# Kernel optimization log

Hardware: AMD Instinct MI355X
Metric: run time of the kernel (lower is better)

## Reference

```python
import jax, jax.numpy as jnp
import numpy as np

EMBED = 768
HEADS = 12


def setup_inputs() -> dict:
    key = jax.random.key(0)
    k1, k2, k3 = jax.random.split(key, 3)
    B, N, E = 2, 2048, EMBED
    x = jax.random.normal(k1, (B, N, E), dtype=jnp.float32)
    w_qkv = jax.random.normal(k2, (3 * E, E), dtype=jnp.float32) * (1.0 / np.sqrt(E))
    b_qkv = jnp.zeros((3 * E,), dtype=jnp.float32)
    w_o = jax.random.normal(k3, (E, E), dtype=jnp.float32) * (1.0 / np.sqrt(E))
    b_o = jnp.zeros((E,), dtype=jnp.float32)
    return {"x": x, "w_qkv": w_qkv, "b_qkv": b_qkv, "w_o": w_o, "b_o": b_o}


def reference(x, w_qkv, b_qkv, w_o, b_o):
    B, N, E = x.shape
    H = HEADS
    d = E // H
    # fused qkv projection (torch Linear: x @ W^T + b)
    qkv = x @ w_qkv.T + b_qkv                       # [B, N, 3E]
    # Rearrange 'b n (h qkv e) -> b qkv h n e'
    qkv = qkv.reshape(B, N, H, 3, d).transpose(0, 3, 2, 1, 4)  # [B, 3, H, N, d]
    q, k, v = qkv[:, 0], qkv[:, 1], qkv[:, 2]       # each [B, H, N, d]
    scores = jnp.einsum("bhqd,bhkd->bhqk", q, k)    # [B, H, N, N]
    attn = jax.nn.softmax(scores / jnp.sqrt(jnp.float32(E)), axis=-1)
    ctx = jnp.einsum("bhqk,bhkd->bhqd", attn, v)    # [B, H, N, d]
    ctx = ctx.transpose(0, 2, 1, 3).reshape(B, N, E)  # 'b h n d -> b n (h d)'
    out = ctx @ w_o.T + b_o
    return out
```

## Files before the change

kernel.cpp:

```cpp
#include <hip/hip_runtime.h>

#define BB 2
#define NN 2048
#define EE 768
#define HH 12
#define DD 64
#define MM (BB*NN)
#define E3 (3*EE)
#define QSCALE 0.05205877280961602f

typedef __bf16 bf16x8 __attribute__((ext_vector_type(8)));
typedef float  f32x4  __attribute__((ext_vector_type(4)));
typedef unsigned short u16x8 __attribute__((ext_vector_type(8)));

#define MFMA(a,b,c) __builtin_amdgcn_mfma_f32_16x16x32_bf16(a,b,c,0,0,0)

__device__ __forceinline__ unsigned short f2bf(float f) {
    unsigned int u = __float_as_uint(f);
    u += 0x7FFFu + ((u >> 16) & 1u);
    return (unsigned short)(u >> 16);
}

typedef __attribute__((address_space(3))) unsigned int as3u32;
typedef __attribute__((address_space(1))) unsigned int as1u32;
__device__ __forceinline__ void gll16(const void* g, void* l) {
    __builtin_amdgcn_global_load_lds((const as1u32*)(uintptr_t)g,
                                     (as3u32*)(unsigned int)(uintptr_t)l, 16, 0, 0);
}

#define XB4 786432
#define WQ4 442368
#define WO4 147456
__global__ __launch_bounds__(256)
void cast3(const float* __restrict__ x, const float* __restrict__ wq,
           const float* __restrict__ wo, unsigned short* __restrict__ dst) {
    int i = blockIdx.x * 256 + threadIdx.x;
    const float* src;
    int off;
    if (i < XB4)            { src = x;  off = i; }
    else if (i < XB4+WQ4)   { src = wq; off = i - XB4; }
    else                    { src = wo; off = i - XB4 - WQ4; }
    float4 v = ((const float4*)src)[off];
    ushort4 o;
    o.x = f2bf(v.x); o.y = f2bf(v.y); o.z = f2bf(v.z); o.w = f2bf(v.w);
    ((ushort4*)dst)[i] = o;
}

__global__ __launch_bounds__(256)
void gemm_qkv(const unsigned short* __restrict__ A, const unsigned short* __restrict__ W,
              const float* __restrict__ bias,
              unsigned short* __restrict__ o0, unsigned short* __restrict__ o1,
              unsigned short* __restrict__ o2)
{
    __shared__ unsigned short As[128 * 32];
    __shared__ unsigned short Bs[64 * 32];

    const int tid = threadIdx.x;
    const int l = tid & 63;
    const int w = tid >> 6;
    const int m0 = blockIdx.x * 128;
    const int c0 = blockIdx.y * 64;
    const int wm = (w >> 1) * 64;
    const int wn = (w & 1) * 32;

    const unsigned short* s_src[3];
    unsigned short* s_dst[3];
    #pragma unroll
    for (int s = 0; s < 3; ++s) {
        const int ch = 3*w + s;
        if (ch < 8) {
            s_src[s] = A + (size_t)(m0 + ch*16 + (l>>2)) * EE + (l&3)*8;
            s_dst[s] = &As[ch*512];
        } else {
            s_src[s] = W + (size_t)(c0 + (ch-8)*16 + (l>>2)) * EE + (l&3)*8;
            s_dst[s] = &Bs[(ch-8)*512];
        }
    }

    const f32x4 zero4 = {0.f, 0.f, 0.f, 0.f};
    f32x4 acc[4][2];
    #pragma unroll
    for (int i = 0; i < 4; ++i)
        #pragma unroll
        for (int j = 0; j < 2; ++j) acc[i][j] = zero4;

    for (int k0 = 0; k0 < EE; k0 += 32) {
        __syncthreads();
        #pragma unroll
        for (int s = 0; s < 3; ++s) gll16(s_src[s] + k0, s_dst[s]);
        __syncthreads();

        bf16x8 af[4], bf[2];
        #pragma unroll
        for (int i = 0; i < 4; ++i)
            af[i] = *(const bf16x8*)&As[(wm + 16*i + (l&15))*32 + (l>>4)*8];
        #pragma unroll
        for (int j = 0; j < 2; ++j)
            bf[j] = *(const bf16x8*)&Bs[(wn + 16*j + (l&15))*32 + (l>>4)*8];
        #pragma unroll
        for (int i = 0; i < 4; ++i)
            #pragma unroll
            for (int j = 0; j < 2; ++j)
                acc[i][j] = MFMA(af[i], bf[j], acc[i][j]);
    }

    const int sec = c0 >> 6;
    const int hh = sec / 3;
    const int tt = sec - hh*3;
    #pragma unroll
    for (int j = 0; j < 2; ++j) {
        const int col = c0 + wn + 16*j + (l&15);
        const int dcol = wn + 16*j + (l&15);
        const float bj = bias[col];
        #pragma unroll
        for (int i = 0; i < 4; ++i) {
            const int row0 = m0 + wm + 16*i + (l>>4)*4;
            const int b = row0 >> 11;
            const int n = row0 & (NN - 1);
            if (tt == 2) {
                ushort4 pk;
                pk.x = f2bf(acc[i][j][0] + bj);
                pk.y = f2bf(acc[i][j][1] + bj);
                pk.z = f2bf(acc[i][j][2] + bj);
                pk.w = f2bf(acc[i][j][3] + bj);
                *(ushort4*)&o2[(((size_t)b*HH + hh)*DD + dcol)*NN + n] = pk;
            } else {
                unsigned short* dst = (tt == 0) ? o0 : o1;
                #pragma unroll
                for (int r = 0; r < 4; ++r) {
                    float val = acc[i][j][r] + bj;
                    if (tt == 0) val *= QSCALE;
                    dst[(((size_t)b*HH + hh)*NN + n + r)*DD + dcol] = f2bf(val);
                }
            }
        }
    }
}

__global__ __launch_bounds__(256)
void gemm_out(const unsigned short* __restrict__ A, const unsigned short* __restrict__ W,
              const float* __restrict__ bias, float* __restrict__ of)
{
    __shared__ unsigned short As[64 * 32];
    __shared__ unsigned short Bs[64 * 32];

    const int tid = threadIdx.x;
    const int l = tid & 63;
    const int w = tid >> 6;
    const int m0 = blockIdx.x * 64;
    const int c0 = blockIdx.y * 64;
    const int wm = (w >> 1) * 32;
    const int wn = (w & 1) * 32;

    const unsigned short* s_src[2];
    unsigned short* s_dst[2];
    #pragma unroll
    for (int s = 0; s < 2; ++s) {
        const int ch = 2*w + s;
        if (ch < 4) {
            s_src[s] = A + (size_t)(m0 + ch*16 + (l>>2)) * EE + (l&3)*8;
            s_dst[s] = &As[ch*512];
        } else {
            s_src[s] = W + (size_t)(c0 + (ch-4)*16 + (l>>2)) * EE + (l&3)*8;
            s_dst[s] = &Bs[(ch-4)*512];
        }
    }

    const f32x4 zero4 = {0.f, 0.f, 0.f, 0.f};
    f32x4 acc[2][2];
    #pragma unroll
    for (int i = 0; i < 2; ++i)
        #pragma unroll
        for (int j = 0; j < 2; ++j) acc[i][j] = zero4;

    for (int k0 = 0; k0 < EE; k0 += 32) {
        __syncthreads();
        #pragma unroll
        for (int s = 0; s < 2; ++s) gll16(s_src[s] + k0, s_dst[s]);
        __syncthreads();

        bf16x8 af[2], bf[2];
        #pragma unroll
        for (int i = 0; i < 2; ++i)
            af[i] = *(const bf16x8*)&As[(wm + 16*i + (l&15))*32 + (l>>4)*8];
        #pragma unroll
        for (int j = 0; j < 2; ++j)
            bf[j] = *(const bf16x8*)&Bs[(wn + 16*j + (l&15))*32 + (l>>4)*8];
        #pragma unroll
        for (int i = 0; i < 2; ++i)
            #pragma unroll
            for (int j = 0; j < 2; ++j)
                acc[i][j] = MFMA(af[i], bf[j], acc[i][j]);
    }

    #pragma unroll
    for (int j = 0; j < 2; ++j) {
        const int col = c0 + wn + 16*j + (l&15);
        const float bj = bias[col];
        #pragma unroll
        for (int i = 0; i < 2; ++i) {
            #pragma unroll
            for (int r = 0; r < 4; ++r) {
                const int row = m0 + wm + 16*i + (l>>4)*4 + r;
                of[(size_t)row * EE + col] = acc[i][j][r] + bj;
            }
        }
    }
}

__global__ __launch_bounds__(256)
void attn_mfma(const unsigned short* __restrict__ Q, const unsigned short* __restrict__ K,
               const unsigned short* __restrict__ Vt_g, unsigned short* __restrict__ ctx)
{
    __shared__ unsigned short Ks[2 * 64 * 64];
    __shared__ unsigned short Vt[2 * 64 * 64];
    __shared__ unsigned short Pq[4 * 2 * 16 * 64];

    const int tid = threadIdx.x;
    const int l = tid & 63;
    const int w = tid >> 6;
    const int quad = l >> 4;
    const int lc = l & 15;
    const int x7 = lc & 7;

    const int id = blockIdx.x;
    const int bh = id % 24;
    const int bq = id / 24;
    const int b  = bh / 12;
    const int h  = bh - b*12;
    const size_t hb = (size_t)bh * NN * DD;

    const f32x4 zero4 = {0.f, 0.f, 0.f, 0.f};

    const int qrow = bq*64 + w*16 + lc;
    const bf16x8 qf0 = *(const bf16x8*)(Q + hb + (size_t)qrow*DD +      quad*8);
    const bf16x8 qf1 = *(const bf16x8*)(Q + hb + (size_t)qrow*DD + 32 + quad*8);

    f32x4 o[4];
    #pragma unroll
    for (int dj = 0; dj < 4; ++dj) o[dj] = zero4;
    float lsum = 0.f;

    const int srow = tid >> 2;
    const int sc = tid & 3;
    const unsigned short* kbase = K + hb + (size_t)srow*DD + sc*16;
    const unsigned short* vbase = Vt_g + hb + (size_t)srow*NN + sc*16;
    const int c0s = ((2*sc)     ^ (srow & 7)) * 8;
    const int c1s = ((2*sc + 1) ^ (srow & 7)) * 8;
    const int so = srow * 64;

    const int chq0 = ((    quad) ^ x7) * 8;
    const int chq1 = ((4 + quad) ^ x7) * 8;
    const int pw = w * 2048;
    const int prd0 = lc*64 + (((    2*quad) ^ (lc & 14)) * 4);
    const int prd1 = lc*64 + (((8 + 2*quad) ^ (lc & 14)) * 4);

    for (int kt = 0; kt < NN/128; ++kt) {
        const unsigned short* k0p = kbase + (size_t)kt*128*DD;
        const unsigned short* k1p = k0p + (size_t)64*DD;
        const unsigned short* v0p = vbase + kt*128;
        const unsigned short* v1p = v0p + 64;
        u16x8 ka0 = *(const u16x8*)k0p;
        u16x8 ka1 = *(const u16x8*)(k0p + 8);
        u16x8 kb0 = *(const u16x8*)k1p;
        u16x8 kb1 = *(const u16x8*)(k1p + 8);
        u16x8 va0 = *(const u16x8*)v0p;
        u16x8 va1 = *(const u16x8*)(v0p + 8);
        u16x8 vb0 = *(const u16x8*)v1p;
        u16x8 vb1 = *(const u16x8*)(v1p + 8);
        __syncthreads();
        *(u16x8*)&Ks[so + c0s] = ka0;
        *(u16x8*)&Ks[so + c1s] = ka1;
        *(u16x8*)&Ks[4096 + so + c0s] = kb0;
        *(u16x8*)&Ks[4096 + so + c1s] = kb1;
        *(u16x8*)&Vt[so + c0s] = va0;
        *(u16x8*)&Vt[so + c1s] = va1;
        *(u16x8*)&Vt[4096 + so + c0s] = vb0;
        *(u16x8*)&Vt[4096 + so + c1s] = vb1;
        __syncthreads();

        #pragma unroll
        for (int hf = 0; hf < 2; ++hf) {
            const int base = hf * 4096;
            const int pb = pw + hf * 1024;

            f32x4 st[4];
            #pragma unroll
            for (int jf = 0; jf < 4; ++jf) {
                bf16x8 kf0 = *(const bf16x8*)&Ks[base + (16*jf + lc)*64 + chq0];
                bf16x8 kf1 = *(const bf16x8*)&Ks[base + (16*jf + lc)*64 + chq1];
                f32x4 acc0 = MFMA(kf0, qf0, zero4);
                st[jf] = MFMA(kf1, qf1, acc0);
            }

            #pragma unroll
            for (int jf = 0; jf < 4; ++jf) {
                float e0 = __builtin_amdgcn_exp2f(st[jf][0]);
                float e1 = __builtin_amdgcn_exp2f(st[jf][1]);
                float e2 = __builtin_amdgcn_exp2f(st[jf][2]);
                float e3 = __builtin_amdgcn_exp2f(st[jf][3]);
                lsum += (e0 + e1) + (e2 + e3);
                ushort4 pk;
                pk.x = f2bf(e0); pk.y = f2bf(e1); pk.z = f2bf(e2); pk.w = f2bf(e3);
                *(ushort4*)&Pq[pb + lc*64 + (((4*jf + quad) ^ (lc & 14)) * 4)] = pk;
            }

            bf16x8 pf0 = *(const bf16x8*)&Pq[pb + prd0];
            bf16x8 pf1 = *(const bf16x8*)&Pq[pb + prd1];
            #pragma unroll
            for (int dj = 0; dj < 4; ++dj) {
                bf16x8 vf0 = *(const bf16x8*)&Vt[base + (16*dj + lc)*64 + chq0];
                bf16x8 vf1 = *(const bf16x8*)&Vt[base + (16*dj + lc)*64 + chq1];
                o[dj] = MFMA(vf0, pf0, o[dj]);
                o[dj] = MFMA(vf1, pf1, o[dj]);
            }
        }
    }

    lsum += __shfl_xor(lsum, 16);
    lsum += __shfl_xor(lsum, 32);
    const float inv = 1.f / lsum;

    const int n = bq*64 + w*16 + lc;
    #pragma unroll
    for (int dj = 0; dj < 4; ++dj) {
        ushort4 pk;
        pk.x = f2bf(o[dj][0] * inv);
        pk.y = f2bf(o[dj][1] * inv);
        pk.z = f2bf(o[dj][2] * inv);
        pk.w = f2bf(o[dj][3] * inv);
        *(ushort4*)&ctx[((size_t)(b*NN + n))*EE + h*DD + 16*dj + quad*4] = pk;
    }
}

extern "C" void kernel_launch(void* const* d_in, const int* in_sizes, int n_in,
                              void* d_out, int out_size, void* d_ws, size_t ws_size,
                              hipStream_t stream)
{
    const float* x     = (const float*)d_in[0];
    const float* w_qkv = (const float*)d_in[1];
    const float* b_qkv = (const float*)d_in[2];
    const float* w_o   = (const float*)d_in[3];
    const float* b_o   = (const float*)d_in[4];
    float* out = (float*)d_out;

    unsigned short* wsu = (unsigned short*)d_ws;
    const size_t XB = (size_t)MM * EE;
    const size_t WQ = (size_t)E3 * EE;
    const size_t WO = (size_t)EE * EE;
    const size_t HS = (size_t)BB * HH * NN * DD;
    unsigned short* xb   = wsu;
    unsigned short* wqb  = xb  + XB;
    unsigned short* wob  = wqb + WQ;
    unsigned short* qb   = wob + WO;
    unsigned short* kb   = qb  + HS;
    unsigned short* vtb  = kb  + HS;
    unsigned short* ctxb = vtb + HS;

    cast3<<<(XB4 + WQ4 + WO4)/256, 256, 0, stream>>>(x, w_qkv, w_o, xb);

    dim3 g1(MM/128, E3/64);
    gemm_qkv<<<g1, 256, 0, stream>>>(xb, wqb, b_qkv, qb, kb, vtb);

    attn_mfma<<<768, 256, 0, stream>>>(qb, kb, vtb, ctxb);

    dim3 g3(MM/64, EE/64);
    gemm_out<<<g3, 256, 0, stream>>>(ctxb, wob, b_o, out);
}
```

Measured before the change: 163.6 us.

## Software-pipeline K/V tile loads into registers across attention iterations

```diff
diff --git a/kernel.cpp b/kernel.cpp
--- a/kernel.cpp
+++ b/kernel.cpp
@@ -208,6 +208,8 @@
     }
 }
 
+struct KVT { u16x8 k0, k1, k2, k3, v0, v1, v2, v3; };
+
 __global__ __launch_bounds__(256)
 void attn_mfma(const unsigned short* __restrict__ Q, const unsigned short* __restrict__ K,
                const unsigned short* __restrict__ Vt_g, unsigned short* __restrict__ ctx)
@@ -255,29 +257,37 @@
     const int prd0 = lc*64 + (((    2*quad) ^ (lc & 14)) * 4);
     const int prd1 = lc*64 + (((8 + 2*quad) ^ (lc & 14)) * 4);
 
-    for (int kt = 0; kt < NN/128; ++kt) {
+    auto loadt = [&](KVT& R, int kt) {
         const unsigned short* k0p = kbase + (size_t)kt*128*DD;
-        const unsigned short* k1p = k0p + (size_t)64*DD;
         const unsigned short* v0p = vbase + kt*128;
-        const unsigned short* v1p = v0p + 64;
-        u16x8 ka0 = *(const u16x8*)k0p;
-        u16x8 ka1 = *(const u16x8*)(k0p + 8);
-        u16x8 kb0 = *(const u16x8*)k1p;
-        u16x8 kb1 = *(const u16x8*)(k1p + 8);
-        u16x8 va0 = *(const u16x8*)v0p;
-        u16x8 va1 = *(const u16x8*)(v0p + 8);
-        u16x8 vb0 = *(const u16x8*)v1p;
-        u16x8 vb1 = *(const u16x8*)(v1p + 8);
-        __syncthreads();
-        *(u16x8*)&Ks[so + c0s] = ka0;
-        *(u16x8*)&Ks[so + c1s] = ka1;
-        *(u16x8*)&Ks[4096 + so + c0s] = kb0;
-        *(u16x8*)&Ks[4096 + so + c1s] = kb1;
-        *(u16x8*)&Vt[so + c0s] = va0;
-        *(u16x8*)&Vt[so + c1s] = va1;
-        *(u16x8*)&Vt[4096 + so + c0s] = vb0;
-        *(u16x8*)&Vt[4096 + so + c1s] = vb1;
-        __syncthreads();
+        R.k0 = *(const u16x8*)k0p;
+        R.k1 = *(const u16x8*)(k0p + 8);
+        R.k2 = *(const u16x8*)(k0p + (size_t)64*DD);
+        R.k3 = *(const u16x8*)(k0p + (size_t)64*DD + 8);
+        R.v0 = *(const u16x8*)v0p;
+        R.v1 = *(const u16x8*)(v0p + 8);
+        R.v2 = *(const u16x8*)(v0p + 64);
+        R.v3 = *(const u16x8*)(v0p + 64 + 8);
+    };
+
+    auto step = [&](KVT& CUR, KVT& NXT, int kt) {
+        asm volatile("s_waitcnt lgkmcnt(0)" ::: "memory");
+        __builtin_amdgcn_s_barrier();
+
+        *(u16x8*)&Ks[so + c0s]        = CUR.k0;
+        *(u16x8*)&Ks[so + c1s]        = CUR.k1;
+        *(u16x8*)&Ks[4096 + so + c0s] = CUR.k2;
+        *(u16x8*)&Ks[4096 + so + c1s] = CUR.k3;
+        *(u16x8*)&Vt[so + c0s]        = CUR.v0;
+        *(u16x8*)&Vt[so + c1s]        = CUR.v1;
+        *(u16x8*)&Vt[4096 + so + c0s] = CUR.v2;
+        *(u16x8*)&Vt[4096 + so + c1s] = CUR.v3;
+
+        if (kt + 1 < NN/128) loadt(NXT, kt + 1);
+
+        asm volatile("s_waitcnt lgkmcnt(0)" ::: "memory");
+        __builtin_amdgcn_s_barrier();
+        __builtin_amdgcn_sched_barrier(0);
 
         #pragma unroll
         for (int hf = 0; hf < 2; ++hf) {
@@ -315,6 +325,13 @@
                 o[dj] = MFMA(vf1, pf1, o[dj]);
             }
         }
+    };
+
+    KVT ra, rb;
+    loadt(ra, 0);
+    for (int it = 0; it < NN/256; ++it) {
+        step(ra, rb, 2*it);
+        step(rb, ra, 2*it + 1);
     }
 
     lsum += __shfl_xor(lsum, 16);
```

After: 170.1 us. +3.9%, slower.
